# Kernel tuning notes

Hardware: AMD Instinct MI355X
Metric: run time of the kernel (lower is better)

The kernel has to match this reference:

```python
import jax, jax.numpy as jnp
import numpy as np

DEPTH = 4      # number of splayers; tplayers = DEPTH-1
SPSIZE = 64
TPSIZE = 32
L = 10.0       # box length
DIM = 3
N = 1024       # number of particles (nup = N//2)
STD = 0.01


def setup_inputs() -> dict:
    key = jax.random.key(0)
    ks = jax.random.split(key, 8)
    tp0 = 2 * DIM + 2                 # tpstream0 feature size = 8
    sp_in0 = 3 * DIM + 2 * tp0        # first f size = 25
    sp_in = 3 * SPSIZE + 2 * TPSIZE   # subsequent f size = 256
    x = jax.random.uniform(ks[0], (N, DIM), jnp.float32, 0.0, L)
    sp_w0 = STD * jax.random.normal(ks[1], (sp_in0, SPSIZE), jnp.float32)
    sp_b0 = jnp.zeros((SPSIZE,), jnp.float32)
    sp_w = STD * jax.random.normal(ks[2], (DEPTH - 1, sp_in, SPSIZE), jnp.float32)
    sp_b = jnp.zeros((DEPTH - 1, SPSIZE), jnp.float32)
    tp_w0 = STD * jax.random.normal(ks[3], (tp0, TPSIZE), jnp.float32)
    tp_b0 = jnp.zeros((TPSIZE,), jnp.float32)
    tp_w = STD * jax.random.normal(ks[4], (DEPTH - 2, TPSIZE, TPSIZE), jnp.float32)
    tp_b = jnp.zeros((DEPTH - 2, TPSIZE), jnp.float32)
    fin_w = STD * jax.random.normal(ks[5], (SPSIZE, DIM), jnp.float32)
    fin_b = jnp.zeros((DIM,), jnp.float32)
    return dict(x=x, sp_w0=sp_w0, sp_b0=sp_b0, sp_w=sp_w, sp_b=sp_b,
                tp_w0=tp_w0, tp_b0=tp_b0, tp_w=tp_w, tp_b=tp_b,
                fin_w=fin_w, fin_b=fin_b)


def _tpstream0(x):
    # pairwise periodic displacement features, shape (n, n, 2*dim+2)
    rij = x[:, None, :] - x[None, :, :]
    c = jnp.cos(2 * jnp.pi / L * rij)
    s = jnp.sin(2 * jnp.pi / L * rij)
    n = x.shape[0]
    eye = jnp.eye(n, dtype=x.dtype)
    dij_sin = jnp.linalg.norm(s + eye[..., None], axis=-1) * (1 - eye)
    dij_cos = jnp.linalg.norm(c + eye[..., None], axis=-1) * (1 - eye)
    return jnp.concatenate((c, s, dij_sin[..., None], dij_cos[..., None]), axis=-1)


def _feat(sp, tp):
    # f = [sp, mean(sp_up), mean(sp_dn), mean_j(tp), mean_i(tp)] -> (n, 3*sp+2*tp)
    n = sp.shape[0]
    nup = n // 2
    up = jnp.broadcast_to(sp[:nup].mean(axis=0, keepdims=True), sp.shape)
    dn = jnp.broadcast_to(sp[nup:].mean(axis=0, keepdims=True), sp.shape)
    return jnp.concatenate((sp, up, dn, tp.mean(axis=1), tp.mean(axis=0)), axis=-1)


def reference(x, sp_w0, sp_b0, sp_w, sp_b, tp_w0, tp_b0, tp_w, tp_b, fin_w, fin_b):
    sp = jnp.zeros_like(x)
    tp = _tpstream0(x)
    for i in range(DEPTH - 1):
        f = _feat(sp, tp)
        w, b = (sp_w0, sp_b0) if i == 0 else (sp_w[i - 1], sp_b[i - 1])
        tw, tb = (tp_w0, tp_b0) if i == 0 else (tp_w[i - 1], tp_b[i - 1])
        sp_new = jax.nn.softplus(f @ w + b)
        tp_new = jax.nn.softplus(tp @ tw + tb)
        sp = sp_new if i == 0 else sp + sp_new
        tp = tp_new if i == 0 else tp + tp_new
    f = _feat(sp, tp)
    sp = sp + jax.nn.softplus(f @ sp_w[DEPTH - 2] + sp_b[DEPTH - 2])
    return x + sp @ fin_w + fin_b
```

## Files before the change

kernel.cpp:

```cpp
#include <hip/hip_runtime.h>

#define NPART 1024
#define NF    104
#define NJS   64
#define NIS   16

typedef __attribute__((ext_vector_type(8))) short short8;
typedef __attribute__((ext_vector_type(4))) float floatx4;

__device__ __forceinline__ float softplus_f(float v) {
    return __logf(1.0f + __expf(v));
}
__device__ __forceinline__ float softplus_p(float a) {
    float t = a * a;
    float h = fmaf(t, 3.4722222e-4f, -5.2083333e-3f);
    h = fmaf(t, h, 0.125f);
    float r = fmaf(a, 0.5f, 0.69314718056f);
    return fmaf(t, h, r);
}
__device__ __forceinline__ unsigned short f2bf(float f) {
    union { float f; unsigned u; } v; v.f = f;
    unsigned r = v.u + 0x7FFFu + ((v.u >> 16) & 1u);
    return (unsigned short)(r >> 16);
}
__device__ __forceinline__ unsigned pk2c(float a, float b) {
    unsigned r;
    asm("v_cvt_pk_bf16_f32 %0, %1, %2" : "=v"(r) : "v"(a), "v"(b));
    return r;
}
__device__ __forceinline__ float bflo(unsigned p) {
    union { unsigned u; float f; } v; v.u = p << 16; return v.f;
}
__device__ __forceinline__ float bfhi(unsigned p) {
    union { unsigned u; float f; } v; v.u = p & 0xffff0000u; return v.f;
}
__device__ __forceinline__ float qsum(float v) {
    v += __shfl_xor(v, 16);
    v += __shfl_xor(v, 32);
    return v;
}

__global__ __launch_bounds__(256) void pair_kernel(
    const float* __restrict__ x,
    const float* __restrict__ tw0, const float* __restrict__ tb0,
    const float* __restrict__ tw,  const float* __restrict__ tb,
    unsigned* __restrict__ ws_rs,
    float* __restrict__ ws_cs,
    float* __restrict__ sums012,
    unsigned* __restrict__ bar)
{
    __shared__ unsigned tpbuf[4][2][320];
    __shared__ float    cmbw[4][16][105];
    __shared__ float4   xjs[16];

    const int t    = threadIdx.x;
    const int w    = t >> 6;
    const int lane = t & 63;
    const int m    = lane & 15;
    const int q    = lane >> 4;
    const int i0   = blockIdx.x * 64;
    const int j0   = blockIdx.y * 16;
    const int ib   = i0 + w * 16;
    const int im   = ib + m;

    if (blockIdx.x == 0 && blockIdx.y == 0 && t < 384) sums012[t] = 0.0f;
    if (blockIdx.x == 0 && blockIdx.y == 0 && t < 4)   bar[t] = 0u;
    if (t < 16) {
        int j = j0 + t;
        xjs[t] = make_float4(x[j * 3], x[j * 3 + 1], x[j * 3 + 2], 0.0f);
    }

    short8 B1[2], B2[2], B3[2];
    float bias1[2], bias2[2], bias3[2];
    #pragma unroll
    for (int nt = 0; nt < 2; ++nt) {
        const int fc = 2 * m + nt;
        bias1[nt] = tb0[fc]; bias2[nt] = tb[fc]; bias3[nt] = tb[32 + fc];
        #pragma unroll
        for (int e = 0; e < 8; ++e) {
            const int k = q * 8 + e;
            B1[nt][e] = (k < 8) ? (short)f2bf(tw0[k * 32 + fc]) : (short)0;
            B2[nt][e] = (short)f2bf(tw[k * 32 + fc]);
            B3[nt][e] = (short)f2bf(tw[1024 + k * 32 + fc]);
        }
    }
    const float xi0 = x[im * 3], xi1 = x[im * 3 + 1], xi2 = x[im * 3 + 2];

    float rowacc1[2][4] = {{0.f,0.f,0.f,0.f},{0.f,0.f,0.f,0.f}};
    float rowacc2[2][4] = {{0.f,0.f,0.f,0.f},{0.f,0.f,0.f,0.f}};
    float rowacc3[2][4] = {{0.f,0.f,0.f,0.f},{0.f,0.f,0.f,0.f}};
    float f0row[8] = {0.f,0.f,0.f,0.f,0.f,0.f,0.f,0.f};

    __syncthreads();

    const float A = 0.62831853071795864769f;
    const floatx4 zero = {0.f, 0.f, 0.f, 0.f};

    #pragma unroll 1
    for (int s = 0; s < 8; ++s) {
        const int jjA = s;
        const int jjB = s + 8;
        float4 xjA = xjs[jjA];
        float4 xjB = xjs[jjB];
        float dA0 = xi0 - xjA.x, dA1 = xi1 - xjA.y, dA2 = xi2 - xjA.z;
        float dB0 = xi0 - xjB.x, dB1 = xi1 - xjB.y, dB2 = xi2 - xjB.z;
        float sA0 = __sinf(A * dA0), sB0 = __sinf(A * dB0);
        float sA1 = __sinf(A * dA1), sB1 = __sinf(A * dB1);
        float sA2 = __sinf(A * dA2), sB2 = __sinf(A * dB2);
        float cA0 = __cosf(A * dA0), cB0 = __cosf(A * dB0);
        float cA1 = __cosf(A * dA1), cB1 = __cosf(A * dB1);
        float cA2 = __cosf(A * dA2), cB2 = __cosf(A * dB2);
        float mkA = (im == j0 + jjA) ? 0.0f : 1.0f;
        float mkB = (im == j0 + jjB) ? 0.0f : 1.0f;
        float dsnA = mkA * sqrtf(sA0 * sA0 + sA1 * sA1 + sA2 * sA2);
        float dsnB = mkB * sqrtf(sB0 * sB0 + sB1 * sB1 + sB2 * sB2);
        float dcsA = mkA * sqrtf(cA0 * cA0 + cA1 * cA1 + cA2 * cA2);
        float dcsB = mkB * sqrtf(cB0 * cB0 + cB1 * cB1 + cB2 * cB2);

        if (q == 0) {
            f0row[0] += cA0 + cB0; f0row[1] += cA1 + cB1; f0row[2] += cA2 + cB2;
            f0row[3] += sA0 + sB0; f0row[4] += sA1 + sB1; f0row[5] += sA2 + sB2;
            f0row[6] += dsnA + dsnB; f0row[7] += dcsA + dcsB;
        }
        uint4 auA = make_uint4(0u, 0u, 0u, 0u);
        uint4 auB = make_uint4(0u, 0u, 0u, 0u);
        if (q == 0) {
            auA = make_uint4(pk2c(cA0, cA1), pk2c(cA2, sA0), pk2c(sA1, sA2), pk2c(dsnA, dcsA));
            auB = make_uint4(pk2c(cB0, cB1), pk2c(cB2, sB0), pk2c(sB1, sB2), pk2c(dsnB, dcsB));
        }
        short8 a1A, a1B;
        *(uint4*)&a1A = auA;
        *(uint4*)&a1B = auB;

        float tpA[2][4], tpB[2][4];
        #pragma unroll
        for (int nt = 0; nt < 2; ++nt) {
            floatx4 ccA = __builtin_amdgcn_mfma_f32_16x16x32_bf16(a1A, B1[nt], zero, 0, 0, 0);
            floatx4 ccB = __builtin_amdgcn_mfma_f32_16x16x32_bf16(a1B, B1[nt], zero, 0, 0, 0);
            float cpA = 0.f, cpB = 0.f;
            #pragma unroll
            for (int r = 0; r < 4; ++r) {
                float vA = softplus_p(ccA[r] + bias1[nt]);
                float vB = softplus_p(ccB[r] + bias1[nt]);
                tpA[nt][r] = vA; tpB[nt][r] = vB;
                rowacc1[nt][r] += vA + vB;
                cpA += vA; cpB += vB;
            }
            cpA = qsum(cpA); cpB = qsum(cpB);
            if (q == 0) {
                cmbw[w][jjA][8 + 2 * m + nt] = cpA;
                cmbw[w][jjB][8 + 2 * m + nt] = cpB;
            }
        }
        #pragma unroll
        for (int r = 0; r < 4; ++r) {
            tpbuf[w][0][(q * 4 + r) * 20 + m] = pk2c(tpA[0][r], tpA[1][r]);
            tpbuf[w][1][(q * 4 + r) * 20 + m] = pk2c(tpB[0][r], tpB[1][r]);
        }
        {
            short8 a2A = *(const short8*)(&tpbuf[w][0][m * 20 + 4 * q]);
            short8 a2B = *(const short8*)(&tpbuf[w][1][m * 20 + 4 * q]);
            #pragma unroll
            for (int nt = 0; nt < 2; ++nt) {
                floatx4 ccA = __builtin_amdgcn_mfma_f32_16x16x32_bf16(a2A, B2[nt], zero, 0, 0, 0);
                floatx4 ccB = __builtin_amdgcn_mfma_f32_16x16x32_bf16(a2B, B2[nt], zero, 0, 0, 0);
                float cpA = 0.f, cpB = 0.f;
                #pragma unroll
                for (int r = 0; r < 4; ++r) {
                    float vA = tpA[nt][r] + softplus_p(ccA[r] + bias2[nt]);
                    float vB = tpB[nt][r] + softplus_p(ccB[r] + bias2[nt]);
                    tpA[nt][r] = vA; tpB[nt][r] = vB;
                    rowacc2[nt][r] += vA + vB;
                    cpA += vA; cpB += vB;
                }
                cpA = qsum(cpA); cpB = qsum(cpB);
                if (q == 0) {
                    cmbw[w][jjA][40 + 2 * m + nt] = cpA;
                    cmbw[w][jjB][40 + 2 * m + nt] = cpB;
                }
            }
            #pragma unroll
            for (int r = 0; r < 4; ++r) {
                tpbuf[w][0][(q * 4 + r) * 20 + m] = pk2c(tpA[0][r], tpA[1][r]);
                tpbuf[w][1][(q * 4 + r) * 20 + m] = pk2c(tpB[0][r], tpB[1][r]);
            }
        }
        {
            short8 a3A = *(const short8*)(&tpbuf[w][0][m * 20 + 4 * q]);
            short8 a3B = *(const short8*)(&tpbuf[w][1][m * 20 + 4 * q]);
            #pragma unroll
            for (int nt = 0; nt < 2; ++nt) {
                floatx4 ccA = __builtin_amdgcn_mfma_f32_16x16x32_bf16(a3A, B3[nt], zero, 0, 0, 0);
                floatx4 ccB = __builtin_amdgcn_mfma_f32_16x16x32_bf16(a3B, B3[nt], zero, 0, 0, 0);
                float cpA = 0.f, cpB = 0.f;
                #pragma unroll
                for (int r = 0; r < 4; ++r) {
                    float vA = tpA[nt][r] + softplus_p(ccA[r] + bias3[nt]);
                    float vB = tpB[nt][r] + softplus_p(ccB[r] + bias3[nt]);
                    rowacc3[nt][r] += vA + vB;
                    cpA += vA; cpB += vB;
                }
                cpA = qsum(cpA); cpB = qsum(cpB);
                if (q == 0) {
                    cmbw[w][jjA][72 + 2 * m + nt] = cpA;
                    cmbw[w][jjB][72 + 2 * m + nt] = cpB;
                }
            }
        }
    }

    unsigned* rbase = ws_rs + (size_t)blockIdx.y * (NPART * 52);
    if (q == 0) {
        #pragma unroll
        for (int e2 = 0; e2 < 4; ++e2)
            rbase[im * 52 + e2] = pk2c(f0row[2 * e2], f0row[2 * e2 + 1]);
    }
    #pragma unroll
    for (int r = 0; r < 4; ++r) {
        const int i = ib + q * 4 + r;
        rbase[i * 52 + 4  + m] = pk2c(rowacc1[0][r], rowacc1[1][r]);
        rbase[i * 52 + 20 + m] = pk2c(rowacc2[0][r], rowacc2[1][r]);
        rbase[i * 52 + 36 + m] = pk2c(rowacc3[0][r], rowacc3[1][r]);
    }
    __syncthreads();
    float* cbase = ws_cs + (size_t)blockIdx.x * (NPART * NF);
    for (int idx = t; idx < 16 * 96; idx += 256) {
        int jj = idx / 96, f = 8 + (idx - jj * 96);
        cbase[(j0 + jj) * NF + f] =
            cmbw[0][jj][f] + cmbw[1][jj][f] + cmbw[2][jj][f] + cmbw[3][jj][f];
    }
}

__device__ __forceinline__ void gridbar(unsigned* bar, int k, unsigned n) {
    __syncthreads();
    if (threadIdx.x == 0) {
        __hip_atomic_fetch_add(&bar[k], 1u, __ATOMIC_RELEASE, __HIP_MEMORY_SCOPE_AGENT);
        while (__hip_atomic_load(&bar[k], __ATOMIC_RELAXED, __HIP_MEMORY_SCOPE_AGENT) < n)
            __builtin_amdgcn_s_sleep(16);
    }
    __syncthreads();
    __builtin_amdgcn_fence(__ATOMIC_ACQUIRE, "agent");
}

__global__ __launch_bounds__(256) void tail_fused(
    const unsigned* __restrict__ ws_rs, const float* __restrict__ ws_cs,
    const float* __restrict__ w0, const float* __restrict__ b0,
    const float* __restrict__ spw, const float* __restrict__ spb,
    const float* __restrict__ x,  const float* __restrict__ finw,
    const float* __restrict__ finb,
    float* __restrict__ sums,
    unsigned* __restrict__ bar,
    float* __restrict__ out)
{
    __shared__ float Srl[16][NF];
    __shared__ float Scl[16][NF];
    __shared__ float sph[16][64];
    __shared__ float uv[64];
    __shared__ float sums_sh[128];
    const int t = threadIdx.x, bid = blockIdx.x;
    const int ty = t >> 6, o = t & 63;
    const int r0 = bid * 16;
    const float sc = 1.0f / 1024.0f;

    for (int u = t; u < 16 * 52; u += 256) {
        int rl = u / 52, uu = u - rl * 52;
        float lo = 0.f, hi = 0.f;
        const unsigned* p = ws_rs + (r0 + rl) * 52 + uu;
        #pragma unroll 16
        for (int s2 = 0; s2 < NJS; ++s2) {
            unsigned v = p[(size_t)s2 * (NPART * 52)];
            lo += bflo(v); hi += bfhi(v);
        }
        Srl[rl][2 * uu] = lo * sc; Srl[rl][2 * uu + 1] = hi * sc;
    }
    __syncthreads();
    for (int u = t; u < 16 * NF; u += 256) {
        int rl = u / NF, f = u - rl * NF;
        float a;
        if (f < 8) {
            float v = Srl[rl][f];
            a = (f >= 3 && f < 6) ? -v : v;
        } else {
            a = 0.f;
            const float* pc = ws_cs + (r0 + rl) * NF + f;
            #pragma unroll
            for (int s2 = 0; s2 < NIS; ++s2) a += pc[(size_t)s2 * (NPART * NF)];
            a *= sc;
        }
        Scl[rl][f] = a;
    }
    __syncthreads();
    #pragma unroll
    for (int rr = ty; rr < 16; rr += 4) {
        float a = b0[o];
        #pragma unroll
        for (int k = 0; k < 8; ++k) a = fmaf(Srl[rr][k], w0[(9 + k) * 64 + o], a);
        #pragma unroll
        for (int k = 0; k < 8; ++k) a = fmaf(Scl[rr][k], w0[(17 + k) * 64 + o], a);
        sph[rr][o] = softplus_f(a);
    }
    __syncthreads();
    if (ty == 0) {
        float ssum = 0.f;
        #pragma unroll
        for (int rr = 0; rr < 16; ++rr) ssum += sph[rr][o];
        atomicAdd(&sums[(bid < 32 ? 0 : 64) + o], ssum);
    }
    gridbar(bar, 0, 64);

    #pragma unroll 1
    for (int st = 0; st < 3; ++st) {
        const float* W  = spw + st * 256 * 64;
        const float* bb = spb + st * 64;
        const int    F0 = 8 + 32 * st;
        if (t < 128)
            sums_sh[t] = __hip_atomic_load(&sums[st * 128 + t],
                                           __ATOMIC_RELAXED, __HIP_MEMORY_SCOPE_AGENT);
        __syncthreads();
        if (t < 64) {
            const float ns = 1.0f / 512.0f;
            float a2 = bb[t];
            #pragma unroll 8
            for (int k = 0; k < 64; ++k) a2 = fmaf(sums_sh[k] * ns, W[(64 + k) * 64 + t], a2);
            #pragma unroll 8
            for (int k = 0; k < 64; ++k) a2 = fmaf(sums_sh[64 + k] * ns, W[(128 + k) * 64 + t], a2);
            uv[t] = a2;
        }
        __syncthreads();
        float nv[4];
        #pragma unroll
        for (int rr4 = 0; rr4 < 4; ++rr4) {
            const int rr = ty + 4 * rr4;
            float a = uv[o];
            #pragma unroll 8
            for (int k = 0; k < 64; ++k) a = fmaf(sph[rr][k], W[k * 64 + o], a);
            #pragma unroll 8
            for (int k = 0; k < 32; ++k) a = fmaf(Srl[rr][F0 + k], W[(192 + k) * 64 + o], a);
            #pragma unroll 8
            for (int k = 0; k < 32; ++k) a = fmaf(Scl[rr][F0 + k], W[(224 + k) * 64 + o], a);
            nv[rr4] = sph[rr][o] + softplus_f(a);
        }
        __syncthreads();
        #pragma unroll
        for (int rr4 = 0; rr4 < 4; ++rr4) sph[ty + 4 * rr4][o] = nv[rr4];
        __syncthreads();
        if (st < 2) {
            if (ty == 0) {
                float ssum = 0.f;
                #pragma unroll
                for (int rr = 0; rr < 16; ++rr) ssum += sph[rr][o];
                atomicAdd(&sums[(st + 1) * 128 + (bid < 32 ? 0 : 64) + o], ssum);
            }
            gridbar(bar, st + 1, 64);
        }
    }

    if (t < 48) {
        int rr = t / 3, d = t - rr * 3;
        int row = r0 + rr;
        float acc = x[row * 3 + d] + finb[d];
        #pragma unroll
        for (int k = 0; k < 64; ++k) acc = fmaf(sph[rr][k], finw[k * 3 + d], acc);
        out[row * 3 + d] = acc;
    }
}

extern "C" void kernel_launch(void* const* d_in, const int* in_sizes, int n_in,
                              void* d_out, int out_size, void* d_ws, size_t ws_size,
                              hipStream_t stream)
{
    (void)in_sizes; (void)n_in; (void)out_size; (void)ws_size;
    const float* x     = (const float*)d_in[0];
    const float* sp_w0 = (const float*)d_in[1];
    const float* sp_b0 = (const float*)d_in[2];
    const float* sp_w  = (const float*)d_in[3];
    const float* sp_b  = (const float*)d_in[4];
    const float* tp_w0 = (const float*)d_in[5];
    const float* tp_b0 = (const float*)d_in[6];
    const float* tp_w  = (const float*)d_in[7];
    const float* tp_b  = (const float*)d_in[8];
    const float* fin_w = (const float*)d_in[9];
    const float* fin_b = (const float*)d_in[10];
    float* out = (float*)d_out;

    unsigned* ws_rs   = (unsigned*)d_ws;
    float*    ws_cs   = (float*)(ws_rs + (size_t)NJS * NPART * 52);
    float*    sums012 = ws_cs + (size_t)NIS * NPART * NF;
    unsigned* bar     = (unsigned*)(sums012 + 384);

    pair_kernel<<<dim3(16, 64), 256, 0, stream>>>(x, tp_w0, tp_b0, tp_w, tp_b,
                                                  ws_rs, ws_cs, sums012, bar);
    tail_fused<<<64, 256, 0, stream>>>(ws_rs, ws_cs, sp_w0, sp_b0,
                                       sp_w, sp_b, x, fin_w, fin_b,
                                       sums012, bar, out);
}
```

Measured before the change: 198.8 us.

## Spread tail kernel over 256 blocks and transpose partial-sum workspace layout

The tail kernel now runs with 256 blocks of 4 rows each instead of 64 blocks of 16, so each thread computes a single row in the dense layers. The partial-sum workspaces are transposed so that each row's partials from all slices sit next to each other, which makes the tail's reduction reads contiguous while the pair kernel's stores become strided. The grid barrier spin sleep is also shortened. In exchange there are more blocks taking part in each grid barrier and more atomic contention on the shared sums, and the weight matrix is reloaded by four times as many blocks.

```diff
diff --git a/kernel.cpp b/kernel.cpp
--- a/kernel.cpp
+++ b/kernel.cpp
@@ -209,24 +209,24 @@
         }
     }
 
-    unsigned* rbase = ws_rs + (size_t)blockIdx.y * (NPART * 52);
+    unsigned* rbase = ws_rs + (size_t)blockIdx.y * 52;
     if (q == 0) {
         #pragma unroll
         for (int e2 = 0; e2 < 4; ++e2)
-            rbase[im * 52 + e2] = pk2c(f0row[2 * e2], f0row[2 * e2 + 1]);
+            rbase[(size_t)im * (NJS * 52) + e2] = pk2c(f0row[2 * e2], f0row[2 * e2 + 1]);
     }
     #pragma unroll
     for (int r = 0; r < 4; ++r) {
-        const int i = ib + q * 4 + r;
-        rbase[i * 52 + 4  + m] = pk2c(rowacc1[0][r], rowacc1[1][r]);
-        rbase[i * 52 + 20 + m] = pk2c(rowacc2[0][r], rowacc2[1][r]);
-        rbase[i * 52 + 36 + m] = pk2c(rowacc3[0][r], rowacc3[1][r]);
-    }
-    __syncthreads();
-    float* cbase = ws_cs + (size_t)blockIdx.x * (NPART * NF);
+        const size_t i = (size_t)(ib + q * 4 + r) * (NJS * 52);
+        rbase[i + 4  + m] = pk2c(rowacc1[0][r], rowacc1[1][r]);
+        rbase[i + 20 + m] = pk2c(rowacc2[0][r], rowacc2[1][r]);
+        rbase[i + 36 + m] = pk2c(rowacc3[0][r], rowacc3[1][r]);
+    }
+    __syncthreads();
+    float* cbase = ws_cs + (size_t)blockIdx.x * NF;
     for (int idx = t; idx < 16 * 96; idx += 256) {
         int jj = idx / 96, f = 8 + (idx - jj * 96);
-        cbase[(j0 + jj) * NF + f] =
+        cbase[(size_t)(j0 + jj) * (NIS * NF) + f] =
             cmbw[0][jj][f] + cmbw[1][jj][f] + cmbw[2][jj][f] + cmbw[3][jj][f];
     }
 }
@@ -236,7 +236,7 @@
     if (threadIdx.x == 0) {
         __hip_atomic_fetch_add(&bar[k], 1u, __ATOMIC_RELEASE, __HIP_MEMORY_SCOPE_AGENT);
         while (__hip_atomic_load(&bar[k], __ATOMIC_RELAXED, __HIP_MEMORY_SCOPE_AGENT) < n)
-            __builtin_amdgcn_s_sleep(16);
+            __builtin_amdgcn_s_sleep(8);
     }
     __syncthreads();
     __builtin_amdgcn_fence(__ATOMIC_ACQUIRE, "agent");
@@ -252,29 +252,29 @@
     unsigned* __restrict__ bar,
     float* __restrict__ out)
 {
-    __shared__ float Srl[16][NF];
-    __shared__ float Scl[16][NF];
-    __shared__ float sph[16][64];
+    __shared__ float Srl[4][NF];
+    __shared__ float Scl[4][NF];
+    __shared__ float sph[4][64];
     __shared__ float uv[64];
     __shared__ float sums_sh[128];
     const int t = threadIdx.x, bid = blockIdx.x;
     const int ty = t >> 6, o = t & 63;
-    const int r0 = bid * 16;
+    const int r0 = bid * 4;
     const float sc = 1.0f / 1024.0f;
 
-    for (int u = t; u < 16 * 52; u += 256) {
+    for (int u = t; u < 4 * 52; u += 256) {
         int rl = u / 52, uu = u - rl * 52;
         float lo = 0.f, hi = 0.f;
-        const unsigned* p = ws_rs + (r0 + rl) * 52 + uu;
+        const unsigned* p = ws_rs + (size_t)(r0 + rl) * (NJS * 52) + uu;
         #pragma unroll 16
         for (int s2 = 0; s2 < NJS; ++s2) {
-            unsigned v = p[(size_t)s2 * (NPART * 52)];
+            unsigned v = p[s2 * 52];
             lo += bflo(v); hi += bfhi(v);
         }
         Srl[rl][2 * uu] = lo * sc; Srl[rl][2 * uu + 1] = hi * sc;
     }
     __syncthreads();
-    for (int u = t; u < 16 * NF; u += 256) {
+    for (int u = t; u < 4 * NF; u += 256) {
         int rl = u / NF, f = u - rl * NF;
         float a;
         if (f < 8) {
@@ -282,31 +282,27 @@
             a = (f >= 3 && f < 6) ? -v : v;
         } else {
             a = 0.f;
-            const float* pc = ws_cs + (r0 + rl) * NF + f;
-            #pragma unroll
-            for (int s2 = 0; s2 < NIS; ++s2) a += pc[(size_t)s2 * (NPART * NF)];
+            const float* pc = ws_cs + (size_t)(r0 + rl) * (NIS * NF) + f;
+            #pragma unroll
+            for (int s2 = 0; s2 < NIS; ++s2) a += pc[s2 * NF];
             a *= sc;
         }
         Scl[rl][f] = a;
     }
     __syncthreads();
-    #pragma unroll
-    for (int rr = ty; rr < 16; rr += 4) {
+    {
         float a = b0[o];
         #pragma unroll
-        for (int k = 0; k < 8; ++k) a = fmaf(Srl[rr][k], w0[(9 + k) * 64 + o], a);
-        #pragma unroll
-        for (int k = 0; k < 8; ++k) a = fmaf(Scl[rr][k], w0[(17 + k) * 64 + o], a);
-        sph[rr][o] = softplus_f(a);
-    }
-    __syncthreads();
-    if (ty == 0) {
-        float ssum = 0.f;
-        #pragma unroll
-        for (int rr = 0; rr < 16; ++rr) ssum += sph[rr][o];
-        atomicAdd(&sums[(bid < 32 ? 0 : 64) + o], ssum);
-    }
-    gridbar(bar, 0, 64);
+        for (int k = 0; k < 8; ++k) a = fmaf(Srl[ty][k], w0[(9 + k) * 64 + o], a);
+        #pragma unroll
+        for (int k = 0; k < 8; ++k) a = fmaf(Scl[ty][k], w0[(17 + k) * 64 + o], a);
+        sph[ty][o] = softplus_f(a);
+    }
+    __syncthreads();
+    if (ty == 0)
+        atomicAdd(&sums[(bid < 128 ? 0 : 64) + o],
+                  sph[0][o] + sph[1][o] + sph[2][o] + sph[3][o]);
+    gridbar(bar, 0, 256);
 
     #pragma unroll 1
     for (int st = 0; st < 3; ++st) {
@@ -327,35 +323,26 @@
             uv[t] = a2;
         }
         __syncthreads();
-        float nv[4];
-        #pragma unroll
-        for (int rr4 = 0; rr4 < 4; ++rr4) {
-            const int rr = ty + 4 * rr4;
-            float a = uv[o];
-            #pragma unroll 8
-            for (int k = 0; k < 64; ++k) a = fmaf(sph[rr][k], W[k * 64 + o], a);
-            #pragma unroll 8
-            for (int k = 0; k < 32; ++k) a = fmaf(Srl[rr][F0 + k], W[(192 + k) * 64 + o], a);
-            #pragma unroll 8
-            for (int k = 0; k < 32; ++k) a = fmaf(Scl[rr][F0 + k], W[(224 + k) * 64 + o], a);
-            nv[rr4] = sph[rr][o] + softplus_f(a);
-        }
+        float a = uv[o];
+        #pragma unroll 8
+        for (int k = 0; k < 64; ++k) a = fmaf(sph[ty][k], W[k * 64 + o], a);
+        #pragma unroll 8
+        for (int k = 0; k < 32; ++k) a = fmaf(Srl[ty][F0 + k], W[(192 + k) * 64 + o], a);
+        #pragma unroll 8
+        for (int k = 0; k < 32; ++k) a = fmaf(Scl[ty][F0 + k], W[(224 + k) * 64 + o], a);
+        float v = sph[ty][o] + softplus_f(a);
         __syncthreads();
-        #pragma unroll
-        for (int rr4 = 0; rr4 < 4; ++rr4) sph[ty + 4 * rr4][o] = nv[rr4];
+        sph[ty][o] = v;
         __syncthreads();
         if (st < 2) {
-            if (ty == 0) {
-                float ssum = 0.f;
-                #pragma unroll
-                for (int rr = 0; rr < 16; ++rr) ssum += sph[rr][o];
-                atomicAdd(&sums[(st + 1) * 128 + (bid < 32 ? 0 : 64) + o], ssum);
-            }
-            gridbar(bar, st + 1, 64);
-        }
-    }
-
-    if (t < 48) {
+            if (ty == 0)
+                atomicAdd(&sums[(st + 1) * 128 + (bid < 128 ? 0 : 64) + o],
+                          sph[0][o] + sph[1][o] + sph[2][o] + sph[3][o]);
+            gridbar(bar, st + 1, 256);
+        }
+    }
+
+    if (t < 12) {
         int rr = t / 3, d = t - rr * 3;
         int row = r0 + rr;
         float acc = x[row * 3 + d] + finb[d];
@@ -384,13 +371,13 @@
     float* out = (float*)d_out;
 
     unsigned* ws_rs   = (unsigned*)d_ws;
-    float*    ws_cs   = (float*)(ws_rs + (size_t)NJS * NPART * 52);
-    float*    sums012 = ws_cs + (size_t)NIS * NPART * NF;
+    float*    ws_cs   = (float*)(ws_rs + (size_t)NPART * NJS * 52);
+    float*    sums012 = ws_cs + (size_t)NPART * NIS * NF;
     unsigned* bar     = (unsigned*)(sums012 + 384);
 
     pair_kernel<<<dim3(16, 64), 256, 0, stream>>>(x, tp_w0, tp_b0, tp_w, tp_b,
                                                   ws_rs, ws_cs, sums012, bar);
-    tail_fused<<<64, 256, 0, stream>>>(ws_rs, ws_cs, sp_w0, sp_b0,
-                                       sp_w, sp_b, x, fin_w, fin_b,
-                                       sums012, bar, out);
-}
+    tail_fused<<<256, 256, 0, stream>>>(ws_rs, ws_cs, sp_w0, sp_b0,
+                                        sp_w, sp_b, x, fin_w, fin_b,
+                                        sums012, bar, out);
+}
```

Result: no change. 201.3 us (+1.3%).
